# Kernel optimization log

Hardware: AMD Instinct MI355X
Metric: run time of the kernel (lower is better)

Reference implementation:

```python
import jax, jax.numpy as jnp
import numpy as np

VOCAB = 50257
H = 1024
T = 4096


def setup_inputs() -> dict:
    key = jax.random.key(0)
    ks = jax.random.split(key, 6)
    scale = 1.0 / np.sqrt(H)  # matches torch LSTM uniform(-1/sqrt(H), 1/sqrt(H)) scale
    return {
        "tokens": jax.random.randint(ks[0], (T,), 0, VOCAB),
        "emb": jax.random.normal(ks[1], (VOCAB, H), dtype=jnp.float32) * 0.02,
        "w_ih": jax.random.uniform(ks[2], (4 * H, H), jnp.float32, -scale, scale),
        "w_hh": jax.random.uniform(ks[3], (4 * H, H), jnp.float32, -scale, scale),
        "b_ih": jax.random.uniform(ks[4], (4 * H,), jnp.float32, -scale, scale),
        "b_hh": jax.random.uniform(ks[5], (4 * H,), jnp.float32, -scale, scale),
    }


def _lstm(x, w_ih, w_hh, b_ih, b_hh):
    # x: [T, H]. Precompute input-side gate projections for all timesteps.
    gx = x @ w_ih.T + (b_ih + b_hh)  # [T, 4H]

    def step(carry, g_t):
        h, c = carry  # [H], [H]
        gates = g_t + h @ w_hh.T  # [4H]
        i, f, g, o = jnp.split(gates, 4)  # torch gate order: input, forget, cell, output
        i = jax.nn.sigmoid(i)
        f = jax.nn.sigmoid(f)
        g = jnp.tanh(g)
        o = jax.nn.sigmoid(o)
        c = f * c + i * g
        h = o * jnp.tanh(c)
        return (h, c), h

    h0 = jnp.zeros((H,), x.dtype)
    c0 = jnp.zeros((H,), x.dtype)
    (h_f, c_f), hs = jax.lax.scan(step, (h0, c0), gx)
    return hs, h_f, c_f  # hs: [T, H]


def reference(tokens, emb, w_ih, w_hh, b_ih, b_hh):
    x = emb[tokens]  # [T, H] embedding lookup
    hs, h_f, c_f = _lstm(x, w_ih, w_hh, b_ih, b_hh)
    output = hs[None, :, :]          # [1, T, H]  (batch_first, batch=1)
    h_n = h_f[None, None, :]         # [1, 1, H]
    c_n = c_f[None, None, :]         # [1, 1, H]
    return (output, (h_n, c_n))
```

## Files before the change

kernel.cpp:

```cpp
#include <hip/hip_runtime.h>
#include <hip/hip_bf16.h>

#define HD   1024
#define GD   4096
#define TT   4096
#define NWG  256

__global__ void embed_kernel(const int* __restrict__ tokens,
                             const float* __restrict__ emb,
                             float* __restrict__ X) {
    int t = blockIdx.x;
    int tok = tokens[t];
    const float4* src = reinterpret_cast<const float4*>(emb + (size_t)tok * HD);
    float4* dst = reinterpret_cast<float4*>(X + (size_t)t * HD);
    dst[threadIdx.x] = src[threadIdx.x];
}

#define BM 128
#define BN 128
#define BK 16
#define LDP 132

__global__ __launch_bounds__(256, 2) void gemm_gx(
    const float* __restrict__ X,
    const float* __restrict__ Wih,
    const float* __restrict__ bih,
    const float* __restrict__ bhh,
    float* __restrict__ gxout)
{
    __shared__ float As[BK][LDP];
    __shared__ float Bs[BK][LDP];
    const int tid = threadIdx.x;
    const int m0 = blockIdx.x * BM;
    const int n0 = blockIdx.y * BN;
    const int tx = tid & 15;
    const int ty = tid >> 4;

    float acc[8][8] = {};

    for (int kt = 0; kt < HD; kt += BK) {
#pragma unroll
        for (int p = 0; p < 2; ++p) {
            int e = p * 256 + tid;
            int row = e >> 2;
            int quad = e & 3;
            float4 av = *reinterpret_cast<const float4*>(
                &X[(size_t)(m0 + row) * HD + kt + quad * 4]);
            float4 bv = *reinterpret_cast<const float4*>(
                &Wih[(size_t)(n0 + row) * HD + kt + quad * 4]);
            As[quad * 4 + 0][row] = av.x;
            As[quad * 4 + 1][row] = av.y;
            As[quad * 4 + 2][row] = av.z;
            As[quad * 4 + 3][row] = av.w;
            Bs[quad * 4 + 0][row] = bv.x;
            Bs[quad * 4 + 1][row] = bv.y;
            Bs[quad * 4 + 2][row] = bv.z;
            Bs[quad * 4 + 3][row] = bv.w;
        }
        __syncthreads();
#pragma unroll
        for (int k = 0; k < BK; ++k) {
            float4 a0 = *reinterpret_cast<const float4*>(&As[k][ty * 8]);
            float4 a1 = *reinterpret_cast<const float4*>(&As[k][ty * 8 + 4]);
            float4 b0 = *reinterpret_cast<const float4*>(&Bs[k][tx * 8]);
            float4 b1 = *reinterpret_cast<const float4*>(&Bs[k][tx * 8 + 4]);
            float a[8] = {a0.x, a0.y, a0.z, a0.w, a1.x, a1.y, a1.z, a1.w};
            float b[8] = {b0.x, b0.y, b0.z, b0.w, b1.x, b1.y, b1.z, b1.w};
#pragma unroll
            for (int i = 0; i < 8; ++i)
#pragma unroll
                for (int j = 0; j < 8; ++j)
                    acc[i][j] += a[i] * b[j];
        }
        __syncthreads();
    }

    float bias[8];
#pragma unroll
    for (int j = 0; j < 8; ++j) {
        int n = n0 + tx * 8 + j;
        bias[j] = bih[n] + bhh[n];
    }
#pragma unroll
    for (int i = 0; i < 8; ++i) {
        size_t o = (size_t)(m0 + ty * 8 + i) * GD + n0 + tx * 8;
        float4 s0 = {acc[i][0] + bias[0], acc[i][1] + bias[1],
                     acc[i][2] + bias[2], acc[i][3] + bias[3]};
        float4 s1 = {acc[i][4] + bias[4], acc[i][5] + bias[5],
                     acc[i][6] + bias[6], acc[i][7] + bias[7]};
        *reinterpret_cast<float4*>(&gxout[o]) = s0;
        *reinterpret_cast<float4*>(&gxout[o + 4]) = s1;
    }
}

__device__ __forceinline__ float sigmoid_(float x) {
    return 1.f / (1.f + __expf(-x));
}
__device__ __forceinline__ float tanh_(float x) {
    return __builtin_fmaf(2.f, 1.f / (1.f + __expf(-2.f * x)), -1.f);
}
__device__ __forceinline__ float bcast_(float v, int l) {
    return __uint_as_float(__builtin_amdgcn_readlane(__float_as_uint(v), l));
}

__global__ __launch_bounds__(256, 1) void lstm_scan(
    const float* __restrict__ gx,
    const float* __restrict__ whh,
    float* __restrict__ out,
    unsigned long long* __restrict__ hbuf)
{
    const int tid   = threadIdx.x;
    const int b     = blockIdx.x;
    const int lane  = tid & 63;
    const int wv    = tid >> 6;
    const int chunk = lane & 15;
    const int gate  = lane >> 4;
    const int j     = b * 4 + wv;
    const int R     = gate * HD + j;

    float w[64];
    {
        const float* wrow = whh + (size_t)R * HD;
#pragma unroll
        for (int q = 0; q < 16; ++q) {
            float4 v = *reinterpret_cast<const float4*>(&wrow[chunk * 4 + q * 64]);
            w[q * 4 + 0] = v.x; w[q * 4 + 1] = v.y;
            w[q * 4 + 2] = v.z; w[q * 4 + 3] = v.w;
        }
    }

    __shared__ float h_lds[2][HD];
#pragma unroll
    for (int q = 0; q < 4; ++q) h_lds[0][tid * 4 + q] = 0.f;
    __syncthreads();

    float c_reg = 0.f;
    float gx_cur = gx[R];

    unsigned long long* const mb[2] = { &hbuf[tid * 4], &hbuf[HD + tid * 4] };

    for (int s = 1; s <= TT; ++s) {
        const int cb = (s - 1) & 1;
        const int nb = s & 1;

        float gx_nxt = 0.f;
        if (s < TT) gx_nxt = gx[(size_t)s * GD + R];

        float acc = (chunk == 0) ? gx_cur : 0.f;
        {
            const float* hb = h_lds[cb];
#pragma unroll
            for (int q = 0; q < 16; ++q) {
                float4 hv = *reinterpret_cast<const float4*>(&hb[chunk * 4 + q * 64]);
                acc = __builtin_fmaf(w[q * 4 + 0], hv.x, acc);
                acc = __builtin_fmaf(w[q * 4 + 1], hv.y, acc);
                acc = __builtin_fmaf(w[q * 4 + 2], hv.z, acc);
                acc = __builtin_fmaf(w[q * 4 + 3], hv.w, acc);
            }
        }
        acc += __shfl_xor(acc, 1, 64);
        acc += __shfl_xor(acc, 2, 64);
        acc += __shfl_xor(acc, 4, 64);
        acc += __shfl_xor(acc, 8, 64);
        float si = bcast_(acc, 0);
        float sf = bcast_(acc, 16);
        float sg = bcast_(acc, 32);
        float so = bcast_(acc, 48);

        float ii = sigmoid_(si);
        float ff = sigmoid_(sf);
        float gg = tanh_(sg);
        float oo = sigmoid_(so);
        c_reg = __builtin_fmaf(ff, c_reg, ii * gg);
        float hh = oo * tanh_(c_reg);

        if (lane == 0) {
            unsigned long long pkt =
                ((unsigned long long)(unsigned)s << 32) | __float_as_uint(hh);
            __hip_atomic_store(&hbuf[(size_t)nb * HD + j], pkt,
                               __ATOMIC_RELAXED, __HIP_MEMORY_SCOPE_AGENT);
            h_lds[nb][j] = hh;
            out[(size_t)(s - 1) * HD + j] = hh;
            if (s == TT) {
                out[(size_t)TT * HD + j] = hh;
                out[(size_t)TT * HD + HD + j] = c_reg;
            }
        }
        gx_cur = gx_nxt;

        if (s < TT) {
            if (tid != b) {
                unsigned long long* src = mb[nb];
                const unsigned long long tag = (unsigned long long)(unsigned)s;
                unsigned long long v0, v1, v2, v3;
                int guard = 0;
                for (;;) {
                    v0 = __hip_atomic_load(&src[0], __ATOMIC_RELAXED,
                                           __HIP_MEMORY_SCOPE_AGENT);
                    v1 = __hip_atomic_load(&src[1], __ATOMIC_RELAXED,
                                           __HIP_MEMORY_SCOPE_AGENT);
                    v2 = __hip_atomic_load(&src[2], __ATOMIC_RELAXED,
                                           __HIP_MEMORY_SCOPE_AGENT);
                    v3 = __hip_atomic_load(&src[3], __ATOMIC_RELAXED,
                                           __HIP_MEMORY_SCOPE_AGENT);
                    bool ok = ((v0 >> 32) == tag) & ((v1 >> 32) == tag) &
                              ((v2 >> 32) == tag) & ((v3 >> 32) == tag);
                    if (ok) break;
                    if (++guard > 4096) {
                        if (guard > (1 << 18)) break;
                        __builtin_amdgcn_s_sleep(1);
                    }
                }
                float4 hv;
                hv.x = __uint_as_float((unsigned int)v0);
                hv.y = __uint_as_float((unsigned int)v1);
                hv.z = __uint_as_float((unsigned int)v2);
                hv.w = __uint_as_float((unsigned int)v3);
                *reinterpret_cast<float4*>(&h_lds[nb][tid * 4]) = hv;
            }
            __syncthreads();
        }
    }
}

extern "C" void kernel_launch(void* const* d_in, const int* in_sizes, int n_in,
                              void* d_out, int out_size, void* d_ws, size_t ws_size,
                              hipStream_t stream) {
    const int*   tokens = (const int*)d_in[0];
    const float* emb    = (const float*)d_in[1];
    const float* w_ih   = (const float*)d_in[2];
    const float* w_hh   = (const float*)d_in[3];
    const float* b_ih   = (const float*)d_in[4];
    const float* b_hh   = (const float*)d_in[5];
    float* out = (float*)d_out;

    char* ws = (char*)d_ws;
    unsigned long long* hbuf = (unsigned long long*)ws;
    float* X  = (float*)(ws + (size_t)16384);
    float* gx = (float*)(ws + (size_t)16384 + (size_t)TT * HD * 4);

    hipMemsetAsync(hbuf, 0, 2 * HD * sizeof(unsigned long long), stream);
    embed_kernel<<<TT, 256, 0, stream>>>(tokens, emb, X);
    gemm_gx<<<dim3(TT / BM, GD / BN), 256, 0, stream>>>(X, w_ih, b_ih, b_hh, gx);
    lstm_scan<<<NWG, 256, 0, stream>>>(gx, w_hh, out, hbuf);
}
```

Baseline: 18.35 ms.

## Fuse embedding into GEMM, pad mailbox slots, split FMA chains, lighten barrier

The embedding gather moves into the GEMM's A-tile load, which removes the separate embed kernel and the intermediate X buffer. In the recurrent scan, each 64-bit h mailbox slot is padded to its own 128-byte stride (MBS=16), so pollers and writers no longer share cache lines. The dot product now uses four independent accumulators to shorten the FMA dependency chain. __syncthreads is replaced by an explicit lgkmcnt wait plus s_barrier, and the LDS/output writes and spin backoff are reordered. This trades more mailbox memory and a memset for fewer cross-block cache-line conflicts on the per-step critical path.

```diff
diff --git a/kernel.cpp b/kernel.cpp
--- a/kernel.cpp
+++ b/kernel.cpp
@@ -5,16 +5,7 @@
 #define GD   4096
 #define TT   4096
 #define NWG  256
-
-__global__ void embed_kernel(const int* __restrict__ tokens,
-                             const float* __restrict__ emb,
-                             float* __restrict__ X) {
-    int t = blockIdx.x;
-    int tok = tokens[t];
-    const float4* src = reinterpret_cast<const float4*>(emb + (size_t)tok * HD);
-    float4* dst = reinterpret_cast<float4*>(X + (size_t)t * HD);
-    dst[threadIdx.x] = src[threadIdx.x];
-}
+#define MBS  16
 
 #define BM 128
 #define BN 128
@@ -22,7 +13,8 @@
 #define LDP 132
 
 __global__ __launch_bounds__(256, 2) void gemm_gx(
-    const float* __restrict__ X,
+    const int* __restrict__ tokens,
+    const float* __restrict__ emb,
     const float* __restrict__ Wih,
     const float* __restrict__ bih,
     const float* __restrict__ bhh,
@@ -36,27 +28,38 @@
     const int tx = tid & 15;
     const int ty = tid >> 4;
 
+    const int quad = tid & 3;
+    const int r0   = tid >> 2;
+    const int tok0 = tokens[m0 + r0];
+    const int tok1 = tokens[m0 + r0 + 64];
+
     float acc[8][8] = {};
 
     for (int kt = 0; kt < HD; kt += BK) {
-#pragma unroll
-        for (int p = 0; p < 2; ++p) {
-            int e = p * 256 + tid;
-            int row = e >> 2;
-            int quad = e & 3;
-            float4 av = *reinterpret_cast<const float4*>(
-                &X[(size_t)(m0 + row) * HD + kt + quad * 4]);
-            float4 bv = *reinterpret_cast<const float4*>(
-                &Wih[(size_t)(n0 + row) * HD + kt + quad * 4]);
-            As[quad * 4 + 0][row] = av.x;
-            As[quad * 4 + 1][row] = av.y;
-            As[quad * 4 + 2][row] = av.z;
-            As[quad * 4 + 3][row] = av.w;
-            Bs[quad * 4 + 0][row] = bv.x;
-            Bs[quad * 4 + 1][row] = bv.y;
-            Bs[quad * 4 + 2][row] = bv.z;
-            Bs[quad * 4 + 3][row] = bv.w;
-        }
+        float4 av0 = *reinterpret_cast<const float4*>(
+            &emb[(size_t)tok0 * HD + kt + quad * 4]);
+        float4 bv0 = *reinterpret_cast<const float4*>(
+            &Wih[(size_t)(n0 + r0) * HD + kt + quad * 4]);
+        float4 av1 = *reinterpret_cast<const float4*>(
+            &emb[(size_t)tok1 * HD + kt + quad * 4]);
+        float4 bv1 = *reinterpret_cast<const float4*>(
+            &Wih[(size_t)(n0 + r0 + 64) * HD + kt + quad * 4]);
+        As[quad * 4 + 0][r0] = av0.x;
+        As[quad * 4 + 1][r0] = av0.y;
+        As[quad * 4 + 2][r0] = av0.z;
+        As[quad * 4 + 3][r0] = av0.w;
+        Bs[quad * 4 + 0][r0] = bv0.x;
+        Bs[quad * 4 + 1][r0] = bv0.y;
+        Bs[quad * 4 + 2][r0] = bv0.z;
+        Bs[quad * 4 + 3][r0] = bv0.w;
+        As[quad * 4 + 0][r0 + 64] = av1.x;
+        As[quad * 4 + 1][r0 + 64] = av1.y;
+        As[quad * 4 + 2][r0 + 64] = av1.z;
+        As[quad * 4 + 3][r0 + 64] = av1.w;
+        Bs[quad * 4 + 0][r0 + 64] = bv1.x;
+        Bs[quad * 4 + 1][r0 + 64] = bv1.y;
+        Bs[quad * 4 + 2][r0 + 64] = bv1.z;
+        Bs[quad * 4 + 3][r0 + 64] = bv1.w;
         __syncthreads();
 #pragma unroll
         for (int k = 0; k < BK; ++k) {
@@ -101,6 +104,10 @@
 }
 __device__ __forceinline__ float bcast_(float v, int l) {
     return __uint_as_float(__builtin_amdgcn_readlane(__float_as_uint(v), l));
+}
+__device__ __forceinline__ void lds_barrier_() {
+    asm volatile("s_waitcnt lgkmcnt(0)" ::: "memory");
+    __builtin_amdgcn_s_barrier();
 }
 
 __global__ __launch_bounds__(256, 1) void lstm_scan(
@@ -132,12 +139,13 @@
     __shared__ float h_lds[2][HD];
 #pragma unroll
     for (int q = 0; q < 4; ++q) h_lds[0][tid * 4 + q] = 0.f;
-    __syncthreads();
+    lds_barrier_();
 
     float c_reg = 0.f;
     float gx_cur = gx[R];
 
-    unsigned long long* const mb[2] = { &hbuf[tid * 4], &hbuf[HD + tid * 4] };
+    unsigned long long* const mp0 = hbuf + (size_t)(tid * 4) * MBS;
+    unsigned long long* const mp1 = hbuf + (size_t)(HD + tid * 4) * MBS;
 
     for (int s = 1; s <= TT; ++s) {
         const int cb = (s - 1) & 1;
@@ -146,18 +154,35 @@
         float gx_nxt = 0.f;
         if (s < TT) gx_nxt = gx[(size_t)s * GD + R];
 
-        float acc = (chunk == 0) ? gx_cur : 0.f;
+        float A0 = (chunk == 0) ? gx_cur : 0.f;
+        float A1 = 0.f, A2 = 0.f, A3 = 0.f;
         {
             const float* hb = h_lds[cb];
 #pragma unroll
-            for (int q = 0; q < 16; ++q) {
-                float4 hv = *reinterpret_cast<const float4*>(&hb[chunk * 4 + q * 64]);
-                acc = __builtin_fmaf(w[q * 4 + 0], hv.x, acc);
-                acc = __builtin_fmaf(w[q * 4 + 1], hv.y, acc);
-                acc = __builtin_fmaf(w[q * 4 + 2], hv.z, acc);
-                acc = __builtin_fmaf(w[q * 4 + 3], hv.w, acc);
-            }
-        }
+            for (int q = 0; q < 4; ++q) {
+                float4 h0 = *reinterpret_cast<const float4*>(&hb[chunk * 4 + (4 * q + 0) * 64]);
+                float4 h1 = *reinterpret_cast<const float4*>(&hb[chunk * 4 + (4 * q + 1) * 64]);
+                float4 h2 = *reinterpret_cast<const float4*>(&hb[chunk * 4 + (4 * q + 2) * 64]);
+                float4 h3 = *reinterpret_cast<const float4*>(&hb[chunk * 4 + (4 * q + 3) * 64]);
+                A0 = __builtin_fmaf(w[(4 * q + 0) * 4 + 0], h0.x, A0);
+                A0 = __builtin_fmaf(w[(4 * q + 0) * 4 + 1], h0.y, A0);
+                A0 = __builtin_fmaf(w[(4 * q + 0) * 4 + 2], h0.z, A0);
+                A0 = __builtin_fmaf(w[(4 * q + 0) * 4 + 3], h0.w, A0);
+                A1 = __builtin_fmaf(w[(4 * q + 1) * 4 + 0], h1.x, A1);
+                A1 = __builtin_fmaf(w[(4 * q + 1) * 4 + 1], h1.y, A1);
+                A1 = __builtin_fmaf(w[(4 * q + 1) * 4 + 2], h1.z, A1);
+                A1 = __builtin_fmaf(w[(4 * q + 1) * 4 + 3], h1.w, A1);
+                A2 = __builtin_fmaf(w[(4 * q + 2) * 4 + 0], h2.x, A2);
+                A2 = __builtin_fmaf(w[(4 * q + 2) * 4 + 1], h2.y, A2);
+                A2 = __builtin_fmaf(w[(4 * q + 2) * 4 + 2], h2.z, A2);
+                A2 = __builtin_fmaf(w[(4 * q + 2) * 4 + 3], h2.w, A2);
+                A3 = __builtin_fmaf(w[(4 * q + 3) * 4 + 0], h3.x, A3);
+                A3 = __builtin_fmaf(w[(4 * q + 3) * 4 + 1], h3.y, A3);
+                A3 = __builtin_fmaf(w[(4 * q + 3) * 4 + 2], h3.z, A3);
+                A3 = __builtin_fmaf(w[(4 * q + 3) * 4 + 3], h3.w, A3);
+            }
+        }
+        float acc = (A0 + A1) + (A2 + A3);
         acc += __shfl_xor(acc, 1, 64);
         acc += __shfl_xor(acc, 2, 64);
         acc += __shfl_xor(acc, 4, 64);
@@ -174,42 +199,35 @@
         c_reg = __builtin_fmaf(ff, c_reg, ii * gg);
         float hh = oo * tanh_(c_reg);
 
-        if (lane == 0) {
-            unsigned long long pkt =
-                ((unsigned long long)(unsigned)s << 32) | __float_as_uint(hh);
-            __hip_atomic_store(&hbuf[(size_t)nb * HD + j], pkt,
-                               __ATOMIC_RELAXED, __HIP_MEMORY_SCOPE_AGENT);
-            h_lds[nb][j] = hh;
-            out[(size_t)(s - 1) * HD + j] = hh;
-            if (s == TT) {
-                out[(size_t)TT * HD + j] = hh;
-                out[(size_t)TT * HD + HD + j] = c_reg;
-            }
-        }
-        gx_cur = gx_nxt;
-
         if (s < TT) {
+            if (lane == 0) {
+                unsigned long long pkt =
+                    ((unsigned long long)(unsigned)s << 32) | __float_as_uint(hh);
+                __hip_atomic_store(&hbuf[(size_t)(nb * HD + j) * MBS], pkt,
+                                   __ATOMIC_RELAXED, __HIP_MEMORY_SCOPE_AGENT);
+            }
+            gx_cur = gx_nxt;
+
             if (tid != b) {
-                unsigned long long* src = mb[nb];
-                const unsigned long long tag = (unsigned long long)(unsigned)s;
+                unsigned long long* src = nb ? mp1 : mp0;
+                const unsigned long long tg = (unsigned long long)(unsigned)s;
                 unsigned long long v0, v1, v2, v3;
-                int guard = 0;
+                int r = 0;
                 for (;;) {
-                    v0 = __hip_atomic_load(&src[0], __ATOMIC_RELAXED,
-                                           __HIP_MEMORY_SCOPE_AGENT);
-                    v1 = __hip_atomic_load(&src[1], __ATOMIC_RELAXED,
-                                           __HIP_MEMORY_SCOPE_AGENT);
-                    v2 = __hip_atomic_load(&src[2], __ATOMIC_RELAXED,
-                                           __HIP_MEMORY_SCOPE_AGENT);
-                    v3 = __hip_atomic_load(&src[3], __ATOMIC_RELAXED,
-                                           __HIP_MEMORY_SCOPE_AGENT);
-                    bool ok = ((v0 >> 32) == tag) & ((v1 >> 32) == tag) &
-                              ((v2 >> 32) == tag) & ((v3 >> 32) == tag);
-                    if (ok) break;
-                    if (++guard > 4096) {
-                        if (guard > (1 << 18)) break;
-                        __builtin_amdgcn_s_sleep(1);
-                    }
+                    v0 = __hip_atomic_load(&src[0 * MBS], __ATOMIC_RELAXED,
+                                           __HIP_MEMORY_SCOPE_AGENT);
+                    v1 = __hip_atomic_load(&src[1 * MBS], __ATOMIC_RELAXED,
+                                           __HIP_MEMORY_SCOPE_AGENT);
+                    v2 = __hip_atomic_load(&src[2 * MBS], __ATOMIC_RELAXED,
+                                           __HIP_MEMORY_SCOPE_AGENT);
+                    v3 = __hip_atomic_load(&src[3 * MBS], __ATOMIC_RELAXED,
+                                           __HIP_MEMORY_SCOPE_AGENT);
+                    unsigned long long bad = ((v0 >> 32) ^ tg) | ((v1 >> 32) ^ tg) |
+                                             ((v2 >> 32) ^ tg) | ((v3 >> 32) ^ tg);
+                    if (!bad) break;
+                    ++r;
+                    if (r > (1 << 17)) break;
+                    if (r >= 2) __builtin_amdgcn_s_sleep(1);
                 }
                 float4 hv;
                 hv.x = __uint_as_float((unsigned int)v0);
@@ -218,7 +236,17 @@
                 hv.w = __uint_as_float((unsigned int)v3);
                 *reinterpret_cast<float4*>(&h_lds[nb][tid * 4]) = hv;
             }
-            __syncthreads();
+            if (lane == 0) {
+                h_lds[nb][j] = hh;
+                out[(size_t)(s - 1) * HD + j] = hh;
+            }
+            lds_barrier_();
+        } else {
+            if (lane == 0) {
+                out[(size_t)(s - 1) * HD + j] = hh;
+                out[(size_t)TT * HD + j] = hh;
+                out[(size_t)TT * HD + HD + j] = c_reg;
+            }
         }
     }
 }
@@ -235,12 +263,12 @@
     float* out = (float*)d_out;
 
     char* ws = (char*)d_ws;
+    const size_t HBUF_BYTES = (size_t)2 * HD * MBS * 8;
     unsigned long long* hbuf = (unsigned long long*)ws;
-    float* X  = (float*)(ws + (size_t)16384);
-    float* gx = (float*)(ws + (size_t)16384 + (size_t)TT * HD * 4);
-
-    hipMemsetAsync(hbuf, 0, 2 * HD * sizeof(unsigned long long), stream);
-    embed_kernel<<<TT, 256, 0, stream>>>(tokens, emb, X);
-    gemm_gx<<<dim3(TT / BM, GD / BN), 256, 0, stream>>>(X, w_ih, b_ih, b_hh, gx);
+    float* gx = (float*)(ws + HBUF_BYTES);
+
+    hipMemsetAsync(hbuf, 0, HBUF_BYTES, stream);
+    gemm_gx<<<dim3(TT / BM, GD / BN), 256, 0, stream>>>(tokens, emb, w_ih,
+                                                        b_ih, b_hh, gx);
     lstm_scan<<<NWG, 256, 0, stream>>>(gx, w_hh, out, hbuf);
 }
```

Result: faster. 16.22 ms (-11.6%).
